# Kernel tuning notes

Hardware: AMD Instinct MI355X
Metric: run time of the kernel (lower is better)

Reference implementation:

```python
import jax, jax.numpy as jnp
import numpy as np
import math

EMB = 2048
NH = 16
HD = EMB // NH
T = 4096
EPS = 1e-5


def setup_inputs() -> dict:
    key = jax.random.key(0)
    ks = jax.random.split(key, 8)
    lim = 1.0 / math.sqrt(EMB)
    q = jax.random.normal(ks[0], (T, EMB), dtype=jnp.float32)
    k = jax.random.normal(ks[1], (T, EMB), dtype=jnp.float32)
    v = jax.random.normal(ks[2], (T, EMB), dtype=jnp.float32)
    Wq = jax.random.uniform(ks[3], (EMB, EMB), minval=-lim, maxval=lim, dtype=jnp.float32)
    Wk = jax.random.uniform(ks[4], (EMB, EMB), minval=-lim, maxval=lim, dtype=jnp.float32)
    Wv = jax.random.uniform(ks[5], (EMB, EMB), minval=-lim, maxval=lim, dtype=jnp.float32)
    Wo = jax.random.uniform(ks[6], (EMB, EMB), minval=-lim, maxval=lim, dtype=jnp.float32)
    ln_w = jnp.ones((EMB,), dtype=jnp.float32)
    mask = jnp.tril(jnp.ones((T, T), dtype=jnp.int32))  # causal
    return {"q": q, "k": k, "v": v, "Wq": Wq, "Wk": Wk, "Wv": Wv,
            "Wo": Wo, "ln_w": ln_w, "mask": mask}


def reference(q, k, v, Wq, Wk, Wv, Wo, ln_w, mask):
    scale = 1.0 / math.sqrt(HD)
    # projections (Linear is weight @ x, i.e. x @ W^T)
    Q = (q @ Wq.T).reshape(T, NH, HD).transpose(1, 0, 2)   # [nh, T, hd]
    K = (k @ Wk.T).reshape(T, NH, HD).transpose(1, 0, 2)
    V = (v @ Wv.T).reshape(T, NH, HD).transpose(1, 0, 2)
    A = jnp.einsum('htd,hsd->hts', Q, K) * scale           # [nh, T, T]
    A = jnp.where(mask != 0, A, -jnp.inf)
    P = jax.nn.softmax(A, axis=-1)
    y = jnp.einsum('hts,hsd->htd', P, V)                   # [nh, T, hd]
    y = y.transpose(1, 0, 2).reshape(T, EMB)               # concat heads
    y = y @ Wo.T
    # deterministic dropout = identity; add residue; per-token LayerNorm (scale only)
    x = y + q
    mu = jnp.mean(x, axis=-1, keepdims=True)
    var = jnp.var(x, axis=-1, keepdims=True)
    return (x - mu) * jax.lax.rsqrt(var + EPS) * ln_w
```

## Files before the change

### kernel.cpp

```cpp
#include <hip/hip_runtime.h>

typedef __bf16 bf16x8 __attribute__((ext_vector_type(8)));
typedef __bf16 bf16x2_t __attribute__((ext_vector_type(2)));
typedef float f32x4 __attribute__((ext_vector_type(4)));
typedef float f32x16 __attribute__((ext_vector_type(16)));
typedef unsigned int u32x4 __attribute__((ext_vector_type(4)));
typedef unsigned short u16x8 __attribute__((ext_vector_type(8)));

#define EMB 2048
#define NH 16
#define HD 128
#define TSEQ 4096

__device__ __forceinline__ unsigned short f2bf(float x) {
  unsigned int u = __builtin_bit_cast(unsigned int, x);
  u += 0x7fffu + ((u >> 16) & 1u);
  return (unsigned short)(u >> 16);
}

__device__ __forceinline__ float bf2f(unsigned short u) {
  unsigned int x = ((unsigned int)u) << 16;
  return __builtin_bit_cast(float, x);
}

__device__ __forceinline__ float ex2(float x) { return __builtin_amdgcn_exp2f(x); }

__device__ __forceinline__ void gl_lds16(const void* g, void* l) {
  __builtin_amdgcn_global_load_lds((__attribute__((address_space(1))) void*)(void*)g,
                                   (__attribute__((address_space(3))) void*)l, 16, 0, 0);
}

template <typename OutT>
__device__ __forceinline__ void store_out(OutT* p, float v) {
  if constexpr (sizeof(OutT) == 2) { *p = f2bf(v); } else { *p = v; }
}

__global__ __launch_bounds__(256) void cvt_all(const float* __restrict__ q, const float* __restrict__ k,
                                               const float* __restrict__ v, const float* __restrict__ Wq,
                                               const float* __restrict__ Wk, const float* __restrict__ Wv,
                                               const float* __restrict__ Wo,
                                               unsigned short* qb, unsigned short* kb, unsigned short* vb,
                                               unsigned short* Wqb, unsigned short* Wkb, unsigned short* Wvb,
                                               unsigned short* Wob) {
  const int SX = TSEQ * EMB / 8;
  const int SW = EMB * EMB / 8;
  int i = blockIdx.x * 256 + threadIdx.x;
  const float* src; unsigned short* dst; int off;
  if (i < 3 * SX) {
    int seg = i >> 20; off = i & (SX - 1);
    src = (seg == 0) ? q : (seg == 1) ? k : v;
    dst = (seg == 0) ? qb : (seg == 1) ? kb : vb;
  } else {
    int j = i - 3 * SX;
    int seg = j >> 19; off = j & (SW - 1);
    src = (seg == 0) ? Wq : (seg == 1) ? Wk : (seg == 2) ? Wv : Wo;
    dst = (seg == 0) ? Wqb : (seg == 1) ? Wkb : (seg == 2) ? Wvb : Wob;
  }
  const float4* p = (const float4*)src + (size_t)off * 2;
  float4 a = p[0], b = p[1];
  u32x4 r;
  r.x = (unsigned)f2bf(a.x) | ((unsigned)f2bf(a.y) << 16);
  r.y = (unsigned)f2bf(a.z) | ((unsigned)f2bf(a.w) << 16);
  r.z = (unsigned)f2bf(b.x) | ((unsigned)f2bf(b.y) << 16);
  r.w = (unsigned)f2bf(b.z) | ((unsigned)f2bf(b.w) << 16);
  ((u32x4*)dst)[off] = r;
}

template <typename OutT>
__device__ __forceinline__ void gemm_body(const unsigned short* __restrict__ A,
                                          const unsigned short* __restrict__ B,
                                          OutT* __restrict__ C,
                                          int m0, int n0, int N, int K, char* smem, float oscale) {
  const int t = threadIdx.x;
  const int l = t & 63, lg = l >> 4, l15 = l & 15;
  const int w = t >> 6, wm = w >> 1, wn = w & 1;

  f32x4 acc[4][4] = {};

  const int rowS = t >> 2;
  const int cbS = (t & 3) * 16;
  const int swS = cbS ^ ((rowS & 3) << 4);
  const char* Ab = (const char*)A + ((size_t)(m0 + rowS) * K) * 2;
  const char* Bb = (const char*)B + ((size_t)(n0 + rowS) * K) * 2;
  const size_t rowStep = (size_t)64 * K * 2;

  auto stage = [&](int buf, int kt) {
    const int ktB = kt * 2;
    char* sA = smem + buf * 8192;
    char* sB = smem + 16384 + buf * 8192;
    gl_lds16(Ab + ktB + swS, sA + t * 16);
    gl_lds16(Ab + rowStep + ktB + swS, sA + 4096 + t * 16);
    gl_lds16(Bb + ktB + swS, sB + t * 16);
    gl_lds16(Bb + rowStep + ktB + swS, sB + 4096 + t * 16);
  };

  const int nIter = K / 32;
  stage(0, 0);
  int cur = 0;
  for (int it = 0; it < nIter; ++it) {
    if (it + 1 < nIter) {
      stage(cur ^ 1, (it + 1) * 32);
      asm volatile("s_waitcnt vmcnt(4)" ::: "memory");
    } else {
      asm volatile("s_waitcnt vmcnt(0)" ::: "memory");
    }
    __builtin_amdgcn_s_barrier();

    const char* sA = smem + cur * 8192;
    const char* sB = smem + 16384 + cur * 8192;
    const int rsw = (l15 & 3) << 4;
    bf16x8 af[4], bfr[4];
#pragma unroll
    for (int m = 0; m < 4; m++) {
      const int r = wm * 64 + m * 16 + l15;
      af[m] = *(const bf16x8*)(sA + r * 64 + ((lg * 16) ^ rsw));
    }
#pragma unroll
    for (int n = 0; n < 4; n++) {
      const int r = wn * 64 + n * 16 + l15;
      bfr[n] = *(const bf16x8*)(sB + r * 64 + ((lg * 16) ^ rsw));
    }
#pragma unroll
    for (int m = 0; m < 4; m++)
#pragma unroll
      for (int n = 0; n < 4; n++)
        acc[m][n] = __builtin_amdgcn_mfma_f32_16x16x32_bf16(af[m], bfr[n], acc[m][n], 0, 0, 0);

    __builtin_amdgcn_s_barrier();
    cur ^= 1;
  }

#pragma unroll
  for (int m = 0; m < 4; m++) {
    int row = m0 + wm * 64 + m * 16 + 4 * lg;
#pragma unroll
    for (int n = 0; n < 4; n++) {
      int col = n0 + wn * 64 + n * 16 + l15;
#pragma unroll
      for (int i = 0; i < 4; i++)
        store_out(C + (size_t)(row + i) * N + col, acc[m][n][i] * oscale);
    }
  }
}

__global__ __launch_bounds__(256) void gemm_qkv(const unsigned short* __restrict__ qb,
                                                const unsigned short* __restrict__ kb,
                                                const unsigned short* __restrict__ vb,
                                                const unsigned short* __restrict__ Wq,
                                                const unsigned short* __restrict__ Wk,
                                                const unsigned short* __restrict__ Wv,
                                                unsigned short* Qo, unsigned short* Ko, unsigned short* Vto) {
  __shared__ char smem[32768];
  const int bx = blockIdx.x;
  const int z = bx >> 9, r = bx & 511;
  const unsigned short* A; const unsigned short* B; unsigned short* C;
  int N, m0, n0; float sc;
  if (z == 0)      { A = qb; B = Wq; C = Qo;  N = EMB;  n0 = (r & 15) << 7; m0 = (r >> 4) << 7; sc = 0.12751743f; }
  else if (z == 1) { A = kb; B = Wk; C = Ko;  N = EMB;  n0 = (r & 15) << 7; m0 = (r >> 4) << 7; sc = 1.0f; }
  else             { A = Wv; B = vb; C = Vto; N = TSEQ; n0 = (r & 31) << 7; m0 = (r >> 5) << 7; sc = 1.0f; }
  gemm_body<unsigned short>(A, B, C, m0, n0, N, EMB, smem, sc);
}

__global__ __launch_bounds__(256) void gemm_o(const unsigned short* __restrict__ A,
                                              const unsigned short* __restrict__ B,
                                              unsigned short* __restrict__ C) {
  __shared__ char smem[32768];
  gemm_body<unsigned short>(A, B, C, blockIdx.y * 128, blockIdx.x * 128, EMB, EMB, smem, 1.0f);
}

__global__ __launch_bounds__(256, 2) void attn_kernel(const unsigned short* __restrict__ Q,
                                                      const unsigned short* __restrict__ Kp,
                                                      const unsigned short* __restrict__ Vt,
                                                      unsigned short* __restrict__ slots,
                                                      float* __restrict__ lbuf) {
  __shared__ char sK[2][16384];
  __shared__ char sV[3][16384];
  const int t = threadIdx.x, l = t & 63, w = t >> 6;
  const int l31 = l & 31, hh = l >> 5;
  const int b = blockIdx.x;
  const int h = b >> 5;
  const int p = (b >> 1) & 15;
  const int half = b & 1;
  const int slotBase = (h * 16 + p) * 3;

  const int q0A = 128 * p, q0B = 128 * (31 - p);
  const int swi = (half == 0) ? (2 * p + 2) : 64;
  const int kvOff = 31 - 2 * p;

  int q0 = (half == 0) ? q0A : q0B;
  int qrow = q0 + w * 32 + l31;

  auto kvof = [&](int gi) -> int {
    if (half == 0) return (gi < swi) ? gi * 64 : (gi - swi) * 64;
    return (kvOff + gi) * 64;
  };

  bf16x8 qf[8];
#pragma unroll
  for (int kd = 0; kd < 8; kd++)
    qf[kd] = *(const bf16x8*)(Q + (size_t)qrow * EMB + h * HD + kd * 16 + hh * 8);

  f32x16 o[4] = {};
  float l_run = 0.0f;

  const int rK = t >> 4, cK = (t & 15) * 16;
  const int rV = t >> 3, cV = (t & 7) * 16;
  const char* Kb = (const char*)Kp;
  const char* Vb = (const char*)Vt;

  auto stage = [&](int kbuf, int vbuf, int kv0) {
#pragma unroll
    for (int c = 0; c < 4; c++) {
      int rowK = c * 16 + rK;
      gl_lds16(Kb + (size_t)(kv0 + rowK) * (EMB * 2) + h * (HD * 2) + (cK ^ ((rowK & 15) << 4)),
               sK[kbuf] + c * 4096 + t * 16);
      int rowV = c * 32 + rV;
      gl_lds16(Vb + (size_t)(h * HD + rowV) * (TSEQ * 2) + kv0 * 2 + (cV ^ ((rowV & 7) << 4)),
               sV[vbuf] + c * 4096 + t * 16);
    }
  };

  auto writeout = [&](int slotId) {
    unsigned short* S = slots + (size_t)slotId * (128 * 128);
    const int r = w * 32 + l31;
    float lt = l_run + __shfl_xor(l_run, 32, 64);
    if (hh == 0) lbuf[slotId * 128 + r] = lt;
#pragma unroll
    for (int hdm = 0; hdm < 4; hdm++)
#pragma unroll
      for (int rq = 0; rq < 4; rq++) {
        ushort4 st;
        st.x = f2bf(o[hdm][4 * rq + 0]);
        st.y = f2bf(o[hdm][4 * rq + 1]);
        st.z = f2bf(o[hdm][4 * rq + 2]);
        st.w = f2bf(o[hdm][4 * rq + 3]);
        *(ushort4*)(S + r * 128 + hdm * 32 + 8 * rq + 4 * hh) = st;
      }
  };

  stage(0, 0, kvof(0));
  int kc = 0, vc = 0, vn = 1;
  for (int gi = 0; gi < 33; ++gi) {
    if (half == 0 && gi == swi) {
      writeout(slotBase + 0);
#pragma unroll
      for (int hdm = 0; hdm < 4; hdm++)
#pragma unroll
        for (int i = 0; i < 16; i++) o[hdm][i] = 0.0f;
      l_run = 0.0f;
      q0 = q0B;
      qrow = q0 + w * 32 + l31;
#pragma unroll
      for (int kd = 0; kd < 8; kd++)
        qf[kd] = *(const bf16x8*)(Q + (size_t)qrow * EMB + h * HD + kd * 16 + hh * 8);
    }
    const int kv0 = kvof(gi);
    if (gi + 1 < 33) {
      stage(kc ^ 1, vn, kvof(gi + 1));
      asm volatile("s_waitcnt vmcnt(8)" ::: "memory");
    } else {
      asm volatile("s_waitcnt vmcnt(0)" ::: "memory");
    }
    __builtin_amdgcn_s_barrier();

    const char* KB = sK[kc];
    const char* VB = sV[vc];

    f32x16 s[2];
#pragma unroll
    for (int i = 0; i < 16; i++) { s[0][i] = -8.0f; s[1][i] = -8.0f; }
    __builtin_amdgcn_s_setprio(1);
#pragma unroll
    for (int kvm = 0; kvm < 2; kvm++) {
      const int rowA = kvm * 32 + l31;
      const int swz = (rowA & 15) << 4;
#pragma unroll
      for (int kd = 0; kd < 8; kd++) {
        bf16x8 kf = *(const bf16x8*)(KB + rowA * 256 + ((kd * 32 + hh * 16) ^ swz));
        s[kvm] = __builtin_amdgcn_mfma_f32_32x32x16_bf16(kf, qf[kd], s[kvm], 0, 0, 0);
      }
    }
    __builtin_amdgcn_s_setprio(0);
    __builtin_amdgcn_s_barrier();

    const bool diag = (kv0 + 64 > q0);
    if (diag) {
#pragma unroll
      for (int kvm = 0; kvm < 2; kvm++)
#pragma unroll
        for (int i = 0; i < 16; i++)
          if (kv0 + kvm * 32 + (i & 3) + 8 * (i >> 2) + 4 * hh > qrow) s[kvm][i] = -1e30f;
    }
    float psum = 0.0f;
    unsigned int wb[16];
#pragma unroll
    for (int kvm = 0; kvm < 2; kvm++)
#pragma unroll
      for (int m = 0; m < 8; m++) {
        float p0 = ex2(s[kvm][2 * m + 0]);
        float p1 = ex2(s[kvm][2 * m + 1]);
        psum += p0 + p1;
        bf16x2_t pk; pk[0] = (__bf16)p0; pk[1] = (__bf16)p1;
        wb[kvm * 8 + m] = __builtin_bit_cast(unsigned int, pk);
      }
    l_run += psum;

    __builtin_amdgcn_s_setprio(1);
#pragma unroll
    for (int kvm = 0; kvm < 2; kvm++)
#pragma unroll
      for (int sx = 0; sx < 2; sx++) {
        const int base = kvm * 8 + 4 * sx;
        const unsigned int a0 = wb[base + 0], a1 = wb[base + 1];
        const unsigned int b0 = wb[base + 2], b1 = wb[base + 3];
        const unsigned int snd0 = hh ? a0 : b0;
        const unsigned int snd1 = hh ? a1 : b1;
        const unsigned int rcv0 = (unsigned int)__shfl_xor((int)snd0, 32, 64);
        const unsigned int rcv1 = (unsigned int)__shfl_xor((int)snd1, 32, 64);
        u32x4 pw;
        pw.x = hh ? rcv0 : a0;
        pw.y = hh ? rcv1 : a1;
        pw.z = hh ? b0 : rcv0;
        pw.w = hh ? b1 : rcv1;
        const bf16x8 pfrag = __builtin_bit_cast(bf16x8, pw);
        const int ks = kvm * 2 + sx;
#pragma unroll
        for (int hdm = 0; hdm < 4; hdm++) {
          const int rowA = hdm * 32 + l31;
          bf16x8 vf = *(const bf16x8*)(VB + rowA * 128 + ((ks * 32 + hh * 16) ^ ((rowA & 7) << 4)));
          o[hdm] = __builtin_amdgcn_mfma_f32_32x32x16_bf16(vf, pfrag, o[hdm], 0, 0, 0);
        }
      }
    __builtin_amdgcn_s_setprio(0);

    kc ^= 1;
    vc = vn;
    vn = (vn == 2) ? 0 : vn + 1;
  }

  writeout(slotBase + ((half == 0) ? 1 : 2));
}

__global__ __launch_bounds__(256) void merge_kernel(const unsigned short* __restrict__ slots,
                                                    const float* __restrict__ lbuf,
                                                    unsigned short* __restrict__ Y) {
  const int tile = blockIdx.x;
  const int h = tile >> 5, tt = tile & 31;
  const int p = (tt <= 15) ? tt : 31 - tt;
  const int base = (h * 16 + p) * 3;
  const int t = threadIdx.x;
  const int r = t >> 1;
  const int c0 = (t & 1) * 64;
  unsigned short* yp = Y + (size_t)(128 * tt + r) * EMB + h * HD + c0;
  if (tt <= 15) {
    const unsigned short* S = slots + (size_t)(base + 0) * (128 * 128) + r * 128 + c0;
    const float inv = 1.0f / lbuf[(base + 0) * 128 + r];
#pragma unroll
    for (int j = 0; j < 8; j++) {
      u16x8 a = ((const u16x8*)S)[j];
      u16x8 ov;
#pragma unroll
      for (int e = 0; e < 8; e++) ov[e] = f2bf(bf2f(a[e]) * inv);
      ((u16x8*)yp)[j] = ov;
    }
  } else {
    const unsigned short* S0 = slots + (size_t)(base + 1) * (128 * 128) + r * 128 + c0;
    const unsigned short* S1 = slots + (size_t)(base + 2) * (128 * 128) + r * 128 + c0;
    const float inv = 1.0f / (lbuf[(base + 1) * 128 + r] + lbuf[(base + 2) * 128 + r]);
#pragma unroll
    for (int j = 0; j < 8; j++) {
      u16x8 a = ((const u16x8*)S0)[j];
      u16x8 c = ((const u16x8*)S1)[j];
      u16x8 ov;
#pragma unroll
      for (int e = 0; e < 8; e++) ov[e] = f2bf((bf2f(a[e]) + bf2f(c[e])) * inv);
      ((u16x8*)yp)[j] = ov;
    }
  }
}

__global__ __launch_bounds__(256) void ln_kernel(const unsigned short* __restrict__ y2,
                                                 const float* __restrict__ qin,
                                                 const float* __restrict__ lnw,
                                                 float* __restrict__ out) {
  const int row = blockIdx.x, t = threadIdx.x;
  const u16x8* Y = (const u16x8*)(y2 + (size_t)row * EMB);
  const float4* Qv = (const float4*)(qin + (size_t)row * EMB);
  u16x8 yv = Y[t];
  float4 b0 = Qv[2 * t], b1 = Qv[2 * t + 1];
  float x[8];
  x[0] = bf2f(yv[0]) + b0.x; x[1] = bf2f(yv[1]) + b0.y;
  x[2] = bf2f(yv[2]) + b0.z; x[3] = bf2f(yv[3]) + b0.w;
  x[4] = bf2f(yv[4]) + b1.x; x[5] = bf2f(yv[5]) + b1.y;
  x[6] = bf2f(yv[6]) + b1.z; x[7] = bf2f(yv[7]) + b1.w;
  float s = 0.0f, s2 = 0.0f;
#pragma unroll
  for (int j = 0; j < 8; j++) { s += x[j]; s2 += x[j] * x[j]; }
#pragma unroll
  for (int d = 1; d < 64; d <<= 1) {
    s += __shfl_xor(s, d, 64);
    s2 += __shfl_xor(s2, d, 64);
  }
  __shared__ float red[8];
  if ((t & 63) == 0) { red[(t >> 6) * 2] = s; red[(t >> 6) * 2 + 1] = s2; }
  __syncthreads();
  s = red[0] + red[2] + red[4] + red[6];
  s2 = red[1] + red[3] + red[5] + red[7];
  float mu = s * (1.0f / EMB);
  float var = s2 * (1.0f / EMB) - mu * mu;
  float r = rsqrtf(var + 1e-5f);
  const float4* Wv4 = (const float4*)lnw;
  float4 w0 = Wv4[2 * t], w1 = Wv4[2 * t + 1];
  float4 o0, o1;
  o0.x = (x[0] - mu) * r * w0.x; o0.y = (x[1] - mu) * r * w0.y;
  o0.z = (x[2] - mu) * r * w0.z; o0.w = (x[3] - mu) * r * w0.w;
  o1.x = (x[4] - mu) * r * w1.x; o1.y = (x[5] - mu) * r * w1.y;
  o1.z = (x[6] - mu) * r * w1.z; o1.w = (x[7] - mu) * r * w1.w;
  ((float4*)(out + (size_t)row * EMB))[2 * t] = o0;
  ((float4*)(out + (size_t)row * EMB))[2 * t + 1] = o1;
}

extern "C" void kernel_launch(void* const* d_in, const int* in_sizes, int n_in,
                              void* d_out, int out_size, void* d_ws, size_t ws_size,
                              hipStream_t stream) {
  const float* q = (const float*)d_in[0];
  const float* k = (const float*)d_in[1];
  const float* v = (const float*)d_in[2];
  const float* Wq = (const float*)d_in[3];
  const float* Wk = (const float*)d_in[4];
  const float* Wv = (const float*)d_in[5];
  const float* Wo = (const float*)d_in[6];
  const float* lnw = (const float*)d_in[7];
  float* out = (float*)d_out;
  char* ws = (char*)d_ws;

  const size_t WB = (size_t)EMB * EMB * 2;
  const size_t XB = (size_t)TSEQ * EMB * 2;
  unsigned short* Wq_b = (unsigned short*)(ws + 0 * WB);
  unsigned short* Wk_b = (unsigned short*)(ws + 1 * WB);
  unsigned short* Wv_b = (unsigned short*)(ws + 2 * WB);
  unsigned short* Wo_b = (unsigned short*)(ws + 3 * WB);
  unsigned short* qb   = (unsigned short*)(ws + 4 * WB);
  unsigned short* kb   = (unsigned short*)(ws + 4 * WB + XB);
  unsigned short* vb   = (unsigned short*)(ws + 4 * WB + 2 * XB);
  unsigned short* Qb   = (unsigned short*)(ws + 4 * WB + 3 * XB);
  unsigned short* Kb   = (unsigned short*)(ws + 4 * WB + 4 * XB);
  unsigned short* Vtb  = (unsigned short*)(ws + 4 * WB + 5 * XB);
  unsigned short* yb   = qb;
  unsigned short* slots = (unsigned short*)(ws + 4 * WB + XB);
  float* lbuf = (float*)(ws + 4 * WB + XB + (size_t)768 * 128 * 128 * 2);
  unsigned short* y2 = (unsigned short*)(ws + 4 * WB + XB);

  cvt_all<<<20480, 256, 0, stream>>>(q, k, v, Wq, Wk, Wv, Wo,
                                     qb, kb, vb, Wq_b, Wk_b, Wv_b, Wo_b);

  gemm_qkv<<<1536, 256, 0, stream>>>(qb, kb, vb, Wq_b, Wk_b, Wv_b, Qb, Kb, Vtb);

  attn_kernel<<<512, 256, 0, stream>>>(Qb, Kb, Vtb, slots, lbuf);

  merge_kernel<<<512, 256, 0, stream>>>(slots, lbuf, yb);

  gemm_o<<<dim3(16, 32), 256, 0, stream>>>(yb, Wo_b, y2);

  ln_kernel<<<TSEQ, 256, 0, stream>>>(y2, q, lnw, out);
}
```

Before: 324.7 us.

## Split causal attention into four KV chunks with 32-wide tiles and higher occupancy

The attention kernel now splits each paired (short + long) causal row-block workload into four equal chunks of 33 KV tiles, each 32 keys wide instead of 64. This doubles the grid to 1024 blocks, halves the LDS per block and raises launch bounds to 4 blocks per SM. The aim is better load balance and more latency hiding across CUs. Partial outputs go to five slots per pair, spread over freed workspace regions. The merge kernel sums a variable number of partial slots per tile. In exchange, each tile does fewer MFMAs between barriers, and there is more partial-output traffic to write and merge.

```diff
diff --git a/kernel.cpp b/kernel.cpp
--- a/kernel.cpp
+++ b/kernel.cpp
@@ -168,31 +168,38 @@
   gemm_body<unsigned short>(A, B, C, blockIdx.y * 128, blockIdx.x * 128, EMB, EMB, smem, 1.0f);
 }
 
-__global__ __launch_bounds__(256, 2) void attn_kernel(const unsigned short* __restrict__ Q,
+__global__ __launch_bounds__(256, 4) void attn_kernel(const unsigned short* __restrict__ Q,
                                                       const unsigned short* __restrict__ Kp,
                                                       const unsigned short* __restrict__ Vt,
-                                                      unsigned short* __restrict__ slots,
+                                                      unsigned short* __restrict__ slotsLo,
+                                                      unsigned short* __restrict__ slotsHi,
                                                       float* __restrict__ lbuf) {
-  __shared__ char sK[2][16384];
-  __shared__ char sV[3][16384];
+  __shared__ char sK[2][8192];
+  __shared__ char sV[3][8192];
   const int t = threadIdx.x, l = t & 63, w = t >> 6;
   const int l31 = l & 31, hh = l >> 5;
   const int b = blockIdx.x;
-  const int h = b >> 5;
-  const int p = (b >> 1) & 15;
-  const int half = b & 1;
-  const int slotBase = (h * 16 + p) * 3;
-
+  const int h = b >> 6;
+  const int p = (b >> 2) & 15;
+  const int chunk = b & 3;
+  const int pairBase = (h * 16 + p) * 5;
+  const int Alen = 4 * p + 4;
+  const int startG = chunk * 33;
   const int q0A = 128 * p, q0B = 128 * (31 - p);
-  const int swi = (half == 0) ? (2 * p + 2) : 64;
-  const int kvOff = 31 - 2 * p;
-
-  int q0 = (half == 0) ? q0A : q0B;
+  const bool startA = (startG < Alen);
+  const int swi = startA ? (Alen - startG) : 999;
+  const bool hasSwitch = startA && (swi < 33);
+
+  int q0 = startA ? q0A : q0B;
   int qrow = q0 + w * 32 + l31;
 
   auto kvof = [&](int gi) -> int {
-    if (half == 0) return (gi < swi) ? gi * 64 : (gi - swi) * 64;
-    return (kvOff + gi) * 64;
+    const int g = startG + gi;
+    return (g < Alen) ? g * 32 : (g - Alen) * 32;
+  };
+
+  auto slotPtr = [&](int s) -> unsigned short* {
+    return (s < 768) ? (slotsLo + (size_t)s * 16384) : (slotsHi + (size_t)(s - 768) * 16384);
   };
 
   bf16x8 qf[8];
@@ -204,24 +211,24 @@
   float l_run = 0.0f;
 
   const int rK = t >> 4, cK = (t & 15) * 16;
-  const int rV = t >> 3, cV = (t & 7) * 16;
+  const int rV = t >> 2, cV = (t & 3) * 16;
   const char* Kb = (const char*)Kp;
   const char* Vb = (const char*)Vt;
 
   auto stage = [&](int kbuf, int vbuf, int kv0) {
 #pragma unroll
-    for (int c = 0; c < 4; c++) {
+    for (int c = 0; c < 2; c++) {
       int rowK = c * 16 + rK;
       gl_lds16(Kb + (size_t)(kv0 + rowK) * (EMB * 2) + h * (HD * 2) + (cK ^ ((rowK & 15) << 4)),
                sK[kbuf] + c * 4096 + t * 16);
-      int rowV = c * 32 + rV;
-      gl_lds16(Vb + (size_t)(h * HD + rowV) * (TSEQ * 2) + kv0 * 2 + (cV ^ ((rowV & 7) << 4)),
+      int rowV = c * 64 + rV;
+      gl_lds16(Vb + (size_t)(h * HD + rowV) * (TSEQ * 2) + kv0 * 2 + (cV ^ ((rowV & 3) << 4)),
                sV[vbuf] + c * 4096 + t * 16);
     }
   };
 
   auto writeout = [&](int slotId) {
-    unsigned short* S = slots + (size_t)slotId * (128 * 128);
+    unsigned short* S = slotPtr(slotId);
     const int r = w * 32 + l31;
     float lt = l_run + __shfl_xor(l_run, 32, 64);
     if (hh == 0) lbuf[slotId * 128 + r] = lt;
@@ -241,8 +248,8 @@
   stage(0, 0, kvof(0));
   int kc = 0, vc = 0, vn = 1;
   for (int gi = 0; gi < 33; ++gi) {
-    if (half == 0 && gi == swi) {
-      writeout(slotBase + 0);
+    if (hasSwitch && gi == swi) {
+      writeout(pairBase + chunk);
 #pragma unroll
       for (int hdm = 0; hdm < 4; hdm++)
 #pragma unroll
@@ -257,7 +264,7 @@
     const int kv0 = kvof(gi);
     if (gi + 1 < 33) {
       stage(kc ^ 1, vn, kvof(gi + 1));
-      asm volatile("s_waitcnt vmcnt(8)" ::: "memory");
+      asm volatile("s_waitcnt vmcnt(4)" ::: "memory");
     } else {
       asm volatile("s_waitcnt vmcnt(0)" ::: "memory");
     }
@@ -266,71 +273,63 @@
     const char* KB = sK[kc];
     const char* VB = sV[vc];
 
-    f32x16 s[2];
-#pragma unroll
-    for (int i = 0; i < 16; i++) { s[0][i] = -8.0f; s[1][i] = -8.0f; }
+    f32x16 s;
+#pragma unroll
+    for (int i = 0; i < 16; i++) s[i] = -8.0f;
     __builtin_amdgcn_s_setprio(1);
-#pragma unroll
-    for (int kvm = 0; kvm < 2; kvm++) {
-      const int rowA = kvm * 32 + l31;
+    {
+      const int rowA = l31;
       const int swz = (rowA & 15) << 4;
 #pragma unroll
       for (int kd = 0; kd < 8; kd++) {
         bf16x8 kf = *(const bf16x8*)(KB + rowA * 256 + ((kd * 32 + hh * 16) ^ swz));
-        s[kvm] = __builtin_amdgcn_mfma_f32_32x32x16_bf16(kf, qf[kd], s[kvm], 0, 0, 0);
+        s = __builtin_amdgcn_mfma_f32_32x32x16_bf16(kf, qf[kd], s, 0, 0, 0);
       }
     }
     __builtin_amdgcn_s_setprio(0);
     __builtin_amdgcn_s_barrier();
 
-    const bool diag = (kv0 + 64 > q0);
+    const bool diag = (kv0 + 32 > q0);
     if (diag) {
 #pragma unroll
-      for (int kvm = 0; kvm < 2; kvm++)
-#pragma unroll
-        for (int i = 0; i < 16; i++)
-          if (kv0 + kvm * 32 + (i & 3) + 8 * (i >> 2) + 4 * hh > qrow) s[kvm][i] = -1e30f;
+      for (int i = 0; i < 16; i++)
+        if (kv0 + (i & 3) + 8 * (i >> 2) + 4 * hh > qrow) s[i] = -1e30f;
     }
     float psum = 0.0f;
-    unsigned int wb[16];
-#pragma unroll
-    for (int kvm = 0; kvm < 2; kvm++)
-#pragma unroll
-      for (int m = 0; m < 8; m++) {
-        float p0 = ex2(s[kvm][2 * m + 0]);
-        float p1 = ex2(s[kvm][2 * m + 1]);
-        psum += p0 + p1;
-        bf16x2_t pk; pk[0] = (__bf16)p0; pk[1] = (__bf16)p1;
-        wb[kvm * 8 + m] = __builtin_bit_cast(unsigned int, pk);
+    unsigned int wb[8];
+#pragma unroll
+    for (int m = 0; m < 8; m++) {
+      float p0 = ex2(s[2 * m + 0]);
+      float p1 = ex2(s[2 * m + 1]);
+      psum += p0 + p1;
+      bf16x2_t pk; pk[0] = (__bf16)p0; pk[1] = (__bf16)p1;
+      wb[m] = __builtin_bit_cast(unsigned int, pk);
+    }
+    l_run += psum;
+
+    __builtin_amdgcn_s_setprio(1);
+#pragma unroll
+    for (int sx = 0; sx < 2; sx++) {
+      const int base = 4 * sx;
+      const unsigned int a0 = wb[base + 0], a1 = wb[base + 1];
+      const unsigned int b0 = wb[base + 2], b1 = wb[base + 3];
+      const unsigned int snd0 = hh ? a0 : b0;
+      const unsigned int snd1 = hh ? a1 : b1;
+      const unsigned int rcv0 = (unsigned int)__shfl_xor((int)snd0, 32, 64);
+      const unsigned int rcv1 = (unsigned int)__shfl_xor((int)snd1, 32, 64);
+      u32x4 pw;
+      pw.x = hh ? rcv0 : a0;
+      pw.y = hh ? rcv1 : a1;
+      pw.z = hh ? b0 : rcv0;
+      pw.w = hh ? b1 : rcv1;
+      const bf16x8 pfrag = __builtin_bit_cast(bf16x8, pw);
+#pragma unroll
+      for (int hdm = 0; hdm < 4; hdm++) {
+        const int rowA = hdm * 32 + l31;
+        bf16x8 vf = *(const bf16x8*)(VB + rowA * 64 + ((sx * 32 + hh * 16) ^ ((rowA & 3) << 4)));
+        o[hdm] = __builtin_amdgcn_mfma_f32_32x32x16_bf16(vf, pfrag, o[hdm], 0, 0, 0);
       }
-    l_run += psum;
-
-    __builtin_amdgcn_s_setprio(1);
-#pragma unroll
-    for (int kvm = 0; kvm < 2; kvm++)
-#pragma unroll
-      for (int sx = 0; sx < 2; sx++) {
-        const int base = kvm * 8 + 4 * sx;
-        const unsigned int a0 = wb[base + 0], a1 = wb[base + 1];
-        const unsigned int b0 = wb[base + 2], b1 = wb[base + 3];
-        const unsigned int snd0 = hh ? a0 : b0;
-        const unsigned int snd1 = hh ? a1 : b1;
-        const unsigned int rcv0 = (unsigned int)__shfl_xor((int)snd0, 32, 64);
-        const unsigned int rcv1 = (unsigned int)__shfl_xor((int)snd1, 32, 64);
-        u32x4 pw;
-        pw.x = hh ? rcv0 : a0;
-        pw.y = hh ? rcv1 : a1;
-        pw.z = hh ? b0 : rcv0;
-        pw.w = hh ? b1 : rcv1;
-        const bf16x8 pfrag = __builtin_bit_cast(bf16x8, pw);
-        const int ks = kvm * 2 + sx;
-#pragma unroll
-        for (int hdm = 0; hdm < 4; hdm++) {
-          const int rowA = hdm * 32 + l31;
-          bf16x8 vf = *(const bf16x8*)(VB + rowA * 128 + ((ks * 32 + hh * 16) ^ ((rowA & 7) << 4)));
-          o[hdm] = __builtin_amdgcn_mfma_f32_32x32x16_bf16(vf, pfrag, o[hdm], 0, 0, 0);
-        }
-      }
+    }
     __builtin_amdgcn_s_setprio(0);
 
     kc ^= 1;
@@ -338,44 +337,50 @@
     vn = (vn == 2) ? 0 : vn + 1;
   }
 
-  writeout(slotBase + ((half == 0) ? 1 : 2));
-}
-
-__global__ __launch_bounds__(256) void merge_kernel(const unsigned short* __restrict__ slots,
+  const bool endA = startA && !hasSwitch;
+  writeout(endA ? (pairBase + chunk) : (pairBase + chunk + 1));
+}
+
+__global__ __launch_bounds__(256) void merge_kernel(const unsigned short* __restrict__ slotsLo,
+                                                    const unsigned short* __restrict__ slotsHi,
                                                     const float* __restrict__ lbuf,
                                                     unsigned short* __restrict__ Y) {
   const int tile = blockIdx.x;
   const int h = tile >> 5, tt = tile & 31;
   const int p = (tt <= 15) ? tt : 31 - tt;
-  const int base = (h * 16 + p) * 3;
+  const int pairBase = (h * 16 + p) * 5;
+  const int cA = (p >= 8) ? 1 : 0;
+  int s0, ns;
+  if (tt <= 15) { s0 = pairBase;          ns = cA + 1; }
+  else          { s0 = pairBase + cA + 1; ns = 4 - cA; }
   const int t = threadIdx.x;
   const int r = t >> 1;
   const int c0 = (t & 1) * 64;
+
+  float lsum = 0.0f;
+  for (int q = 0; q < ns; q++) lsum += lbuf[(s0 + q) * 128 + r];
+  const float inv = 1.0f / lsum;
+
+  const unsigned short* Sp[4];
+  for (int q = 0; q < ns; q++) {
+    const int s = s0 + q;
+    Sp[q] = ((s < 768) ? (slotsLo + (size_t)s * 16384) : (slotsHi + (size_t)(s - 768) * 16384))
+            + r * 128 + c0;
+  }
+
   unsigned short* yp = Y + (size_t)(128 * tt + r) * EMB + h * HD + c0;
-  if (tt <= 15) {
-    const unsigned short* S = slots + (size_t)(base + 0) * (128 * 128) + r * 128 + c0;
-    const float inv = 1.0f / lbuf[(base + 0) * 128 + r];
-#pragma unroll
-    for (int j = 0; j < 8; j++) {
-      u16x8 a = ((const u16x8*)S)[j];
-      u16x8 ov;
-#pragma unroll
-      for (int e = 0; e < 8; e++) ov[e] = f2bf(bf2f(a[e]) * inv);
-      ((u16x8*)yp)[j] = ov;
-    }
-  } else {
-    const unsigned short* S0 = slots + (size_t)(base + 1) * (128 * 128) + r * 128 + c0;
-    const unsigned short* S1 = slots + (size_t)(base + 2) * (128 * 128) + r * 128 + c0;
-    const float inv = 1.0f / (lbuf[(base + 1) * 128 + r] + lbuf[(base + 2) * 128 + r]);
-#pragma unroll
-    for (int j = 0; j < 8; j++) {
-      u16x8 a = ((const u16x8*)S0)[j];
-      u16x8 c = ((const u16x8*)S1)[j];
-      u16x8 ov;
-#pragma unroll
-      for (int e = 0; e < 8; e++) ov[e] = f2bf((bf2f(a[e]) + bf2f(c[e])) * inv);
-      ((u16x8*)yp)[j] = ov;
-    }
+#pragma unroll
+  for (int j = 0; j < 8; j++) {
+    float acc8[8] = {};
+    for (int q = 0; q < ns; q++) {
+      u16x8 a = ((const u16x8*)Sp[q])[j];
+#pragma unroll
+      for (int e = 0; e < 8; e++) acc8[e] += bf2f(a[e]);
+    }
+    u16x8 ov;
+#pragma unroll
+    for (int e = 0; e < 8; e++) ov[e] = f2bf(acc8[e] * inv);
+    ((u16x8*)yp)[j] = ov;
   }
 }
 
@@ -447,18 +452,19 @@
   unsigned short* Kb   = (unsigned short*)(ws + 4 * WB + 4 * XB);
   unsigned short* Vtb  = (unsigned short*)(ws + 4 * WB + 5 * XB);
   unsigned short* yb   = qb;
-  unsigned short* slots = (unsigned short*)(ws + 4 * WB + XB);
-  float* lbuf = (float*)(ws + 4 * WB + XB + (size_t)768 * 128 * 128 * 2);
-  unsigned short* y2 = (unsigned short*)(ws + 4 * WB + XB);
+  unsigned short* slotsLo = (unsigned short*)(ws);
+  unsigned short* slotsHi = (unsigned short*)(ws + 4 * WB + XB);
+  float* lbuf = (float*)(ws + 4 * WB + 2 * XB);
+  unsigned short* y2 = Qb;
 
   cvt_all<<<20480, 256, 0, stream>>>(q, k, v, Wq, Wk, Wv, Wo,
                                      qb, kb, vb, Wq_b, Wk_b, Wv_b, Wo_b);
 
   gemm_qkv<<<1536, 256, 0, stream>>>(qb, kb, vb, Wq_b, Wk_b, Wv_b, Qb, Kb, Vtb);
 
-  attn_kernel<<<512, 256, 0, stream>>>(Qb, Kb, Vtb, slots, lbuf);
-
-  merge_kernel<<<512, 256, 0, stream>>>(slots, lbuf, yb);
+  attn_kernel<<<1024, 256, 0, stream>>>(Qb, Kb, Vtb, slotsLo, slotsHi, lbuf);
+
+  merge_kernel<<<512, 256, 0, stream>>>(slotsLo, slotsHi, lbuf, yb);
 
   gemm_o<<<dim3(16, 32), 256, 0, stream>>>(yb, Wo_b, y2);
 
```

New measurement: 511.3 us. 1.57x slower.
